# Kernel optimization log

Measured on AMD Instinct MI355X. Metric: run time of the kernel, lower is better.

## Reference

```python
import jax, jax.numpy as jnp
import numpy as np

INPUT_SIZE = 2048
HIDDEN_SIZE = 2048
BATCH = 8192


def setup_inputs() -> dict:
    key = jax.random.key(0)
    ks = jax.random.split(key, 8)
    comb = INPUT_SIZE + HIDDEN_SIZE
    s = 1.0 / np.sqrt(comb)  # torch nn.Linear default init scale
    x = jax.random.normal(ks[0], (BATCH, INPUT_SIZE), dtype=jnp.float32)
    h_prev = jax.random.normal(ks[1], (BATCH, HIDDEN_SIZE), dtype=jnp.float32)
    W_z = jax.random.uniform(ks[2], (comb, HIDDEN_SIZE), minval=-s, maxval=s, dtype=jnp.float32)
    b_z = jax.random.uniform(ks[3], (HIDDEN_SIZE,), minval=-s, maxval=s, dtype=jnp.float32)
    W_r = jax.random.uniform(ks[4], (comb, HIDDEN_SIZE), minval=-s, maxval=s, dtype=jnp.float32)
    b_r = jax.random.uniform(ks[5], (HIDDEN_SIZE,), minval=-s, maxval=s, dtype=jnp.float32)
    W_n = jax.random.uniform(ks[6], (comb, HIDDEN_SIZE), minval=-s, maxval=s, dtype=jnp.float32)
    b_n = jax.random.uniform(ks[7], (HIDDEN_SIZE,), minval=-s, maxval=s, dtype=jnp.float32)
    return {"x": x, "h_prev": h_prev, "W_z": W_z, "b_z": b_z,
            "W_r": W_r, "b_r": b_r, "W_n": W_n, "b_n": b_n}


def reference(x, h_prev, W_z, b_z, W_r, b_r, W_n, b_n):
    # combined = [x, h_prev]; avoid materializing concat by splitting the
    # weight matrices: W @ concat == x @ W_x + h @ W_h (same math).
    Wz_x, Wz_h = W_z[:INPUT_SIZE], W_z[INPUT_SIZE:]
    Wr_x, Wr_h = W_r[:INPUT_SIZE], W_r[INPUT_SIZE:]
    Wn_x, Wn_h = W_n[:INPUT_SIZE], W_n[INPUT_SIZE:]
    z = jax.nn.sigmoid(x @ Wz_x + h_prev @ Wz_h + b_z)
    r = jax.nn.sigmoid(x @ Wr_x + h_prev @ Wr_h + b_r)
    n = jnp.tanh(x @ Wn_x + (r * h_prev) @ Wn_h + b_n)
    h = (1.0 - z) * h_prev + z * n
    return h
```

## Files before the change

### kernel.cpp

```cpp
#include <hip/hip_runtime.h>
#include <hip/hip_bf16.h>
#include <stdint.h>

typedef unsigned short u16;
typedef __attribute__((ext_vector_type(8))) __bf16 bf16x8;
typedef __attribute__((ext_vector_type(4))) float f32x4;

#define BATCH 8192
#define HID   2048
#define COMB  4096
#define NT    64

__device__ __forceinline__ u16 f2bf(float f) {
  uint32_t u = __float_as_uint(f);
  u += 0x7fffu + ((u >> 16) & 1u);
  return (u16)(u >> 16);
}
__device__ __forceinline__ float bf2f(u16 b) {
  return __uint_as_float(((uint32_t)b) << 16);
}
__device__ __forceinline__ float fsigmoid(float x) { return 1.0f / (1.0f + __expf(-x)); }
__device__ __forceinline__ float ftanh(float x) { return 1.0f - 2.0f / (__expf(2.0f * x) + 1.0f); }

__device__ __forceinline__ void gload_lds16(const void* g, void* l) {
  __builtin_amdgcn_global_load_lds(
      (__attribute__((address_space(1))) void*)(uintptr_t)g,
      (__attribute__((address_space(3))) void*)(uintptr_t)l,
      16, 0, 0);
}

#define BARRIER() do { asm volatile("" ::: "memory"); __builtin_amdgcn_s_barrier(); asm volatile("" ::: "memory"); } while (0)
#define LGKM0()   asm volatile("s_waitcnt lgkmcnt(0)" ::: "memory")
#define VM6()     asm volatile("s_waitcnt vmcnt(6)" ::: "memory")
#define VM0()     asm volatile("s_waitcnt vmcnt(0)" ::: "memory")

__device__ __forceinline__ void stage_half(const u16* __restrict__ src, size_t ld,
                                           char* ldsHalf, int w, int l) {
  const int lrow = l >> 3;
  const int g    = (l & 7) ^ (lrow & 7);
#pragma unroll
  for (int i = 0; i < 2; ++i) {
    const int r0 = (w * 2 + i) * 8;
    gload_lds16(src + (size_t)(r0 + lrow) * ld + g * 8, ldsHalf + r0 * 128);
  }
}

__device__ __forceinline__ bf16x8 rd(const char* buf, int row, int kk) {
  const int byte = row * 128 + ((((kk >> 3) & 7) ^ (row & 7)) << 4);
  return *(const bf16x8*)(buf + byte);
}

#define MFMA_QUAD(MH, NH)                                                          \
  {                                                                                \
    _Pragma("unroll") for (int m_ = 0; m_ < 4; ++m_) {                             \
      _Pragma("unroll") for (int n_ = 0; n_ < 2; ++n_) {                           \
        _Pragma("unroll") for (int ks_ = 0; ks_ < 2; ++ks_) {                      \
          acc[(MH)*4 + m_][(NH)*2 + n_] = __builtin_amdgcn_mfma_f32_16x16x32_bf16( \
              af[(MH)*4 + m_][ks_], bb[(NH)*2 + n_][ks_],                          \
              acc[(MH)*4 + m_][(NH)*2 + n_], 0, 0, 0);                             \
        } } }                                                                      \
  }

__global__ void pack_A_kernel(const float* __restrict__ x, const float* __restrict__ h,
                              u16* __restrict__ A1) {
  const size_t tid = (size_t)blockIdx.x * blockDim.x + threadIdx.x;
  const int r  = (int)(tid >> 9);
  const int c8 = (int)(tid & 511);
  const float* s = (c8 < 256) ? (x + (size_t)r * 2048 + (size_t)c8 * 8)
                              : (h + (size_t)r * 2048 + (size_t)(c8 - 256) * 8);
  const float4 v0 = ((const float4*)s)[0];
  const float4 v1 = ((const float4*)s)[1];
  const uint32_t p0 = (uint32_t)f2bf(v0.x) | ((uint32_t)f2bf(v0.y) << 16);
  const uint32_t p1 = (uint32_t)f2bf(v0.z) | ((uint32_t)f2bf(v0.w) << 16);
  const uint32_t p2 = (uint32_t)f2bf(v1.x) | ((uint32_t)f2bf(v1.y) << 16);
  const uint32_t p3 = (uint32_t)f2bf(v1.z) | ((uint32_t)f2bf(v1.w) << 16);
  *(uint4*)(A1 + tid * 8) = make_uint4(p0, p1, p2, p3);
}

__global__ void transpose_w_kernel(const float* __restrict__ src, u16* __restrict__ dst) {
  __shared__ float tile[32][33];
  const int n0 = blockIdx.x * 32;
  const int k0 = blockIdx.y * 32;
  const int tx = threadIdx.x, ty = threadIdx.y;
#pragma unroll
  for (int i = 0; i < 32; i += 8)
    tile[ty + i][tx] = src[(size_t)(k0 + ty + i) * 2048 + n0 + tx];
  __syncthreads();
#pragma unroll
  for (int i = 0; i < 32; i += 8)
    dst[(size_t)(n0 + ty + i) * 4096 + k0 + tx] = f2bf(tile[tx][ty + i]);
}

template <int MODE>
__global__ __launch_bounds__(512, 2) void gemm8p_kernel(
    const u16* __restrict__ A1, const u16* __restrict__ RH,
    const u16* __restrict__ Bt, const float* __restrict__ h_prev,
    const float* __restrict__ bias0, const float* __restrict__ bias1,
    u16* __restrict__ Z, u16* __restrict__ RHout, float* __restrict__ out) {
  extern __shared__ char smem[];
  constexpr int NBN = (MODE == 0) ? 16 : 8;

  const int t = threadIdx.x;
  const int l = t & 63, w = t >> 6;
  const int wm = w >> 2, wn = w & 3;
  const int lr = l & 15, khi = l >> 4;

  const int nwg = 32 * NBN;
  int bid = blockIdx.x;
  bid = (bid & 7) * (nwg >> 3) + (bid >> 3);
  const int bm = bid / NBN, bn = bid % NBN;
  const int arow = bm * 256;
  const int brow = bn * 256;

  char* Abase = smem;
  char* Bbase = smem + 65536;

  auto stageA = [&](int T, int half) {
    const u16* src;
    size_t ld;
    if constexpr (MODE == 1) {
      if (T >= 32) { src = RH + (size_t)(arow + half * 128) * HID + (T * 64 - 2048); ld = HID; }
      else         { src = A1 + (size_t)(arow + half * 128) * COMB + T * 64;         ld = COMB; }
    } else {
      src = A1 + (size_t)(arow + half * 128) * COMB + T * 64; ld = COMB;
    }
    stage_half(src, ld, Abase + (((T & 1) * 2 + half) << 14), w, l);
  };
  auto stageB = [&](int T, int half) {
    stage_half(Bt + (size_t)(brow + half * 128) * COMB + T * 64, COMB,
               Bbase + (((T & 1) * 2 + half) << 14), w, l);
  };

  stageA(0, 0); stageA(0, 1); stageB(0, 0); stageB(0, 1);
  stageA(1, 0); stageA(1, 1); stageB(1, 0);
  VM6();
  BARRIER();

  f32x4 acc[8][4] = {};
  bf16x8 af[8][2], bb[4][2];

#pragma unroll 2
  for (int j = 0; j < NT; ++j) {
    const int p = j & 1;
    const char* Ah = Abase + (((p << 1) + wm) << 14);
    const char* Bh = Bbase + (((p << 1) + (wn >> 1)) << 14);
    const int bro = (wn & 1) * 64;

#pragma unroll
    for (int m = 0; m < 8; ++m)
#pragma unroll
      for (int ks = 0; ks < 2; ++ks)
        af[m][ks] = rd(Ah, m * 16 + lr, ks * 32 + khi * 8);
#pragma unroll
    for (int n = 0; n < 2; ++n)
#pragma unroll
      for (int ks = 0; ks < 2; ++ks)
        bb[n][ks] = rd(Bh, bro + n * 16 + lr, ks * 32 + khi * 8);
    if (j < NT - 1) stageB(j + 1, 1);
    BARRIER();
    LGKM0();
    __builtin_amdgcn_s_setprio(1);
    MFMA_QUAD(0, 0);
    __builtin_amdgcn_s_setprio(0);
    BARRIER();

    if (j < NT - 2) stageA(j + 2, 0);
    BARRIER();
    __builtin_amdgcn_s_setprio(1);
    MFMA_QUAD(1, 0);
    __builtin_amdgcn_s_setprio(0);
    BARRIER();

#pragma unroll
    for (int n = 2; n < 4; ++n)
#pragma unroll
      for (int ks = 0; ks < 2; ++ks)
        bb[n][ks] = rd(Bh, bro + n * 16 + lr, ks * 32 + khi * 8);
    if (j < NT - 2) stageA(j + 2, 1);
    BARRIER();
    LGKM0();
    __builtin_amdgcn_s_setprio(1);
    MFMA_QUAD(1, 1);
    __builtin_amdgcn_s_setprio(0);
    BARRIER();

    if (j < NT - 2) stageB(j + 2, 0);
    BARRIER();
    __builtin_amdgcn_s_setprio(1);
    MFMA_QUAD(0, 1);
    __builtin_amdgcn_s_setprio(0);
    if (j < NT - 2) { VM6(); } else { VM0(); }
    BARRIER();
  }

  const int r0g = arow + wm * 128 + khi * 4;
  const int c0g = brow + wn * 64 + lr;
  if constexpr (MODE == 0) {
    const bool isZ = (bn < 8);
    const float* bias = isZ ? bias0 : bias1;
#pragma unroll
    for (int n = 0; n < 4; ++n) {
      const int colg = c0g + n * 16;
      const int col = isZ ? colg : (colg - 2048);
      const float bv = bias[col];
#pragma unroll
      for (int m = 0; m < 8; ++m)
#pragma unroll
        for (int r = 0; r < 4; ++r) {
          const int row = r0g + m * 16 + r;
          const size_t idx = (size_t)row * HID + col;
          const float v = acc[m][n][r] + bv;
          if (isZ) {
            Z[idx] = f2bf(fsigmoid(v));
          } else {
            const float rv = fsigmoid(v);
            RHout[idx] = f2bf(rv * h_prev[idx]);
          }
        }
    }
  } else {
#pragma unroll
    for (int n = 0; n < 4; ++n) {
      const int col = c0g + n * 16;
      const float bv = bias0[col];
#pragma unroll
      for (int m = 0; m < 8; ++m)
#pragma unroll
        for (int r = 0; r < 4; ++r) {
          const int row = r0g + m * 16 + r;
          const size_t idx = (size_t)row * HID + col;
          const float nn = ftanh(acc[m][n][r] + bv);
          const float zz = bf2f(Z[idx]);
          const float hp = h_prev[idx];
          out[idx] = (1.0f - zz) * hp + zz * nn;
        }
    }
  }
}

extern "C" void kernel_launch(void* const* d_in, const int* in_sizes, int n_in,
                              void* d_out, int out_size, void* d_ws, size_t ws_size,
                              hipStream_t stream) {
  const float* x  = (const float*)d_in[0];
  const float* h  = (const float*)d_in[1];
  const float* Wz = (const float*)d_in[2];
  const float* bz = (const float*)d_in[3];
  const float* Wr = (const float*)d_in[4];
  const float* br = (const float*)d_in[5];
  const float* Wn = (const float*)d_in[6];
  const float* bn = (const float*)d_in[7];
  float* out = (float*)d_out;

  char* ws = (char*)d_ws;
  u16* A1  = (u16*)(ws);
  u16* RH  = (u16*)(ws + 67108864);
  u16* B1t = (u16*)(ws + 100663296);
  u16* B2t = (u16*)(ws + 134217728);
  u16* Z   = (u16*)(ws + 150994944);

  (void)hipFuncSetAttribute(reinterpret_cast<const void*>(&gemm8p_kernel<0>),
                            hipFuncAttributeMaxDynamicSharedMemorySize, 131072);
  (void)hipFuncSetAttribute(reinterpret_cast<const void*>(&gemm8p_kernel<1>),
                            hipFuncAttributeMaxDynamicSharedMemorySize, 131072);

  pack_A_kernel<<<16384, 256, 0, stream>>>(x, h, A1);
  dim3 tb(32, 8);
  transpose_w_kernel<<<dim3(64, 128), tb, 0, stream>>>(Wz, B1t);
  transpose_w_kernel<<<dim3(64, 128), tb, 0, stream>>>(Wr, B1t + (size_t)2048 * 4096);
  transpose_w_kernel<<<dim3(64, 128), tb, 0, stream>>>(Wn, B2t);

  gemm8p_kernel<0><<<dim3(512), 512, 131072, stream>>>(A1, nullptr, B1t, h, bz, br, Z, RH, nullptr);
  gemm8p_kernel<1><<<dim3(256), 512, 131072, stream>>>(A1, RH, B2t, h, bn, nullptr, Z, nullptr, out);
}
```

Measured before the change: 581.5 us.

## Prefetch next-tile LDS fragments during MFMA and relax waitcnts in GEMM loop

Restructures the main GEMM loop so A and B fragments for the next k-tile are read from LDS while MFMAs on the current tile run, using split lo/hi register fragments and a peeled final iteration. The loop now waits on lgkmcnt(8) rather than lgkmcnt(0), and global-to-LDS staging is reordered with finer vmcnt waits. Addressing is simplified by precomputing swizzled lane offsets. The aim is to hide LDS read latency behind matrix work, at the cost of more live registers and tighter synchronisation that could introduce races.

```diff
diff --git a/kernel.cpp b/kernel.cpp
--- a/kernel.cpp
+++ b/kernel.cpp
@@ -30,9 +30,10 @@
 }
 
 #define BARRIER() do { asm volatile("" ::: "memory"); __builtin_amdgcn_s_barrier(); asm volatile("" ::: "memory"); } while (0)
-#define LGKM0()   asm volatile("s_waitcnt lgkmcnt(0)" ::: "memory")
-#define VM6()     asm volatile("s_waitcnt vmcnt(6)" ::: "memory")
-#define VM0()     asm volatile("s_waitcnt vmcnt(0)" ::: "memory")
+#define LGKM8()   asm volatile("s_waitcnt lgkmcnt(8)" ::: "memory")
+#define VMCNT2()  asm volatile("s_waitcnt vmcnt(2)" ::: "memory")
+#define VMCNT0()  asm volatile("s_waitcnt vmcnt(0)" ::: "memory")
+#define VMCNT6()  asm volatile("s_waitcnt vmcnt(6)" ::: "memory")
 
 __device__ __forceinline__ void stage_half(const u16* __restrict__ src, size_t ld,
                                            char* ldsHalf, int w, int l) {
@@ -45,21 +46,16 @@
   }
 }
 
-__device__ __forceinline__ bf16x8 rd(const char* buf, int row, int kk) {
-  const int byte = row * 128 + ((((kk >> 3) & 7) ^ (row & 7)) << 4);
-  return *(const bf16x8*)(buf + byte);
-}
-
-#define MFMA_QUAD(MH, NH)                                                          \
-  {                                                                                \
-    _Pragma("unroll") for (int m_ = 0; m_ < 4; ++m_) {                             \
-      _Pragma("unroll") for (int n_ = 0; n_ < 2; ++n_) {                           \
-        _Pragma("unroll") for (int ks_ = 0; ks_ < 2; ++ks_) {                      \
-          acc[(MH)*4 + m_][(NH)*2 + n_] = __builtin_amdgcn_mfma_f32_16x16x32_bf16( \
-              af[(MH)*4 + m_][ks_], bb[(NH)*2 + n_][ks_],                          \
-              acc[(MH)*4 + m_][(NH)*2 + n_], 0, 0, 0);                             \
-        } } }                                                                      \
-  }
+#define RDA(base, m, ks) (*(const bf16x8*)((base) + ((ks) ? loff1 : loff0) + (m) * 2048))
+#define RDB(base, n, ks) (*(const bf16x8*)((base) + ((ks) ? loff1 : loff0) + (n) * 2048))
+
+#define MFMA_HALF(AF, BB, MH, NH)                                                     \
+  { _Pragma("unroll") for (int m_ = 0; m_ < 4; ++m_) {                                \
+      _Pragma("unroll") for (int n_ = 0; n_ < 2; ++n_) {                              \
+        _Pragma("unroll") for (int k_ = 0; k_ < 2; ++k_) {                            \
+          acc[(MH) * 4 + m_][(NH) * 2 + n_] = __builtin_amdgcn_mfma_f32_16x16x32_bf16(\
+              AF[m_][k_], BB[n_][k_], acc[(MH) * 4 + m_][(NH) * 2 + n_], 0, 0, 0);    \
+        } } } }
 
 __global__ void pack_A_kernel(const float* __restrict__ x, const float* __restrict__ h,
                               u16* __restrict__ A1) {
@@ -131,67 +127,79 @@
                Bbase + (((T & 1) * 2 + half) << 14), w, l);
   };
 
+  const int loff0 = lr * 128 + (((khi)     ^ (lr & 7)) << 4);
+  const int loff1 = lr * 128 + (((4 + khi) ^ (lr & 7)) << 4);
+  const char* A0p = Abase + ((0 * 2 + wm) << 14);
+  const char* A1p = Abase + ((1 * 2 + wm) << 14);
+  const char* B0p = Bbase + ((0 * 2 + (wn >> 1)) << 14) + (wn & 1) * 64 * 128;
+  const char* B1p = Bbase + ((1 * 2 + (wn >> 1)) << 14) + (wn & 1) * 64 * 128;
+
   stageA(0, 0); stageA(0, 1); stageB(0, 0); stageB(0, 1);
-  stageA(1, 0); stageA(1, 1); stageB(1, 0);
-  VM6();
+  stageB(1, 0); stageB(1, 1); stageA(1, 0);
+  VMCNT6();
   BARRIER();
 
   f32x4 acc[8][4] = {};
-  bf16x8 af[8][2], bb[4][2];
+  bf16x8 af_lo[4][2], af_hi[4][2], bb_lo[2][2], bb_hi[2][2];
+
+#pragma unroll
+  for (int m = 0; m < 4; ++m) { af_lo[m][0] = RDA(A0p, m, 0); af_lo[m][1] = RDA(A0p, m, 1); }
+#pragma unroll
+  for (int n = 0; n < 2; ++n) { bb_hi[n][0] = RDB(B0p, n + 2, 0); bb_hi[n][1] = RDB(B0p, n + 2, 1); }
+#pragma unroll
+  for (int n = 0; n < 2; ++n) { bb_lo[n][0] = RDB(B0p, n, 0); bb_lo[n][1] = RDB(B0p, n, 1); }
 
 #pragma unroll 2
-  for (int j = 0; j < NT; ++j) {
-    const int p = j & 1;
-    const char* Ah = Abase + (((p << 1) + wm) << 14);
-    const char* Bh = Bbase + (((p << 1) + (wn >> 1)) << 14);
-    const int bro = (wn & 1) * 64;
-
-#pragma unroll
-    for (int m = 0; m < 8; ++m)
-#pragma unroll
-      for (int ks = 0; ks < 2; ++ks)
-        af[m][ks] = rd(Ah, m * 16 + lr, ks * 32 + khi * 8);
-#pragma unroll
-    for (int n = 0; n < 2; ++n)
-#pragma unroll
-      for (int ks = 0; ks < 2; ++ks)
-        bb[n][ks] = rd(Bh, bro + n * 16 + lr, ks * 32 + khi * 8);
-    if (j < NT - 1) stageB(j + 1, 1);
-    BARRIER();
-    LGKM0();
-    __builtin_amdgcn_s_setprio(1);
-    MFMA_QUAD(0, 0);
+  for (int j = 0; j < NT - 1; ++j) {
+    const bool odd = j & 1;
+    const char* Acur = odd ? A1p : A0p;
+    const char* Anxt = odd ? A0p : A1p;
+    const char* Bnxt = odd ? B0p : B1p;
+
+    stageA(j + 1, 1);
+    BARRIER();
+#pragma unroll
+    for (int m = 0; m < 4; ++m) { af_hi[m][0] = RDA(Acur, m + 4, 0); af_hi[m][1] = RDA(Acur, m + 4, 1); }
+    __builtin_amdgcn_s_setprio(1);
+    MFMA_HALF(af_lo, bb_lo, 0, 0);
+    __builtin_amdgcn_s_setprio(0);
+    LGKM8();
+    BARRIER();
+
+    if (j < NT - 2) stageB(j + 2, 0);
+    BARRIER();
+    __builtin_amdgcn_s_setprio(1);
+    MFMA_HALF(af_lo, bb_hi, 0, 1);
+    __builtin_amdgcn_s_setprio(0);
+    BARRIER();
+
+    if (j < NT - 2) { VMCNT2(); stageB(j + 2, 1); } else { VMCNT0(); }
+    BARRIER();
+#pragma unroll
+    for (int m = 0; m < 4; ++m) { af_lo[m][0] = RDA(Anxt, m, 0); af_lo[m][1] = RDA(Anxt, m, 1); }
+    __builtin_amdgcn_s_setprio(1);
+    MFMA_HALF(af_hi, bb_hi, 1, 1);
     __builtin_amdgcn_s_setprio(0);
     BARRIER();
 
     if (j < NT - 2) stageA(j + 2, 0);
     BARRIER();
-    __builtin_amdgcn_s_setprio(1);
-    MFMA_QUAD(1, 0);
-    __builtin_amdgcn_s_setprio(0);
-    BARRIER();
-
-#pragma unroll
-    for (int n = 2; n < 4; ++n)
-#pragma unroll
-      for (int ks = 0; ks < 2; ++ks)
-        bb[n][ks] = rd(Bh, bro + n * 16 + lr, ks * 32 + khi * 8);
-    if (j < NT - 2) stageA(j + 2, 1);
-    BARRIER();
-    LGKM0();
-    __builtin_amdgcn_s_setprio(1);
-    MFMA_QUAD(1, 1);
-    __builtin_amdgcn_s_setprio(0);
-    BARRIER();
-
-    if (j < NT - 2) stageB(j + 2, 0);
-    BARRIER();
-    __builtin_amdgcn_s_setprio(1);
-    MFMA_QUAD(0, 1);
-    __builtin_amdgcn_s_setprio(0);
-    if (j < NT - 2) { VM6(); } else { VM0(); }
+#pragma unroll
+    for (int n = 0; n < 2; ++n) { bb_hi[n][0] = RDB(Bnxt, n + 2, 0); bb_hi[n][1] = RDB(Bnxt, n + 2, 1); }
+    __builtin_amdgcn_s_setprio(1);
+    MFMA_HALF(af_hi, bb_lo, 1, 0);
+    __builtin_amdgcn_s_setprio(0);
+#pragma unroll
+    for (int n = 0; n < 2; ++n) { bb_lo[n][0] = RDB(Bnxt, n, 0); bb_lo[n][1] = RDB(Bnxt, n, 1); }
     BARRIER();
   }
+
+#pragma unroll
+  for (int m = 0; m < 4; ++m) { af_hi[m][0] = RDA(A1p, m + 4, 0); af_hi[m][1] = RDA(A1p, m + 4, 1); }
+  MFMA_HALF(af_lo, bb_lo, 0, 0);
+  MFMA_HALF(af_lo, bb_hi, 0, 1);
+  MFMA_HALF(af_hi, bb_hi, 1, 1);
+  MFMA_HALF(af_hi, bb_lo, 1, 0);
 
   const int r0g = arow + wm * 128 + khi * 4;
   const int c0g = brow + wn * 64 + lr;
```

After: 679.0 us. 1.17x slower.

## Split A-fragment LDS reads and A staging across MFMA phases with precomputed offsets

Applied to the files above, without the earlier changes.

The LDS reads of the A fragments are split so half are loaded before the first MFMA quad and half before the second, rather than all up front. The A global-to-LDS staging is reissued as quarter-tile loads, spread over two phases and covering both halves, instead of whole halves in separate phases. Swizzled LDS offsets are precomputed once per thread, and a partial lgkmcnt wait is added before the first barrier. The aim is to spread LDS and VMEM traffic more evenly across the MFMA phases and cut address arithmetic, at the cost of reordering which buffer regions are written when, which could risk hazards or extra stalls.

```diff
diff --git a/kernel.cpp b/kernel.cpp
--- a/kernel.cpp
+++ b/kernel.cpp
@@ -31,6 +31,7 @@
 
 #define BARRIER() do { asm volatile("" ::: "memory"); __builtin_amdgcn_s_barrier(); asm volatile("" ::: "memory"); } while (0)
 #define LGKM0()   asm volatile("s_waitcnt lgkmcnt(0)" ::: "memory")
+#define LGKM8()   asm volatile("s_waitcnt lgkmcnt(8)" ::: "memory")
 #define VM6()     asm volatile("s_waitcnt vmcnt(6)" ::: "memory")
 #define VM0()     asm volatile("s_waitcnt vmcnt(0)" ::: "memory")
 
@@ -45,9 +46,12 @@
   }
 }
 
-__device__ __forceinline__ bf16x8 rd(const char* buf, int row, int kk) {
-  const int byte = row * 128 + ((((kk >> 3) & 7) ^ (row & 7)) << 4);
-  return *(const bf16x8*)(buf + byte);
+__device__ __forceinline__ void stage_q(const u16* __restrict__ src, size_t ld,
+                                        char* ldsHalf, int q, int w, int l) {
+  const int lrow = l >> 3;
+  const int g    = (l & 7) ^ (lrow & 7);
+  const int r0   = q * 64 + w * 8;
+  gload_lds16(src + (size_t)(r0 + lrow) * ld + g * 8, ldsHalf + r0 * 128);
 }
 
 #define MFMA_QUAD(MH, NH)                                                          \
@@ -115,24 +119,31 @@
   char* Abase = smem;
   char* Bbase = smem + 65536;
 
-  auto stageA = [&](int T, int half) {
-    const u16* src;
-    size_t ld;
+  auto asrc = [&](int T, int half) -> const u16* {
     if constexpr (MODE == 1) {
-      if (T >= 32) { src = RH + (size_t)(arow + half * 128) * HID + (T * 64 - 2048); ld = HID; }
-      else         { src = A1 + (size_t)(arow + half * 128) * COMB + T * 64;         ld = COMB; }
-    } else {
-      src = A1 + (size_t)(arow + half * 128) * COMB + T * 64; ld = COMB;
-    }
-    stage_half(src, ld, Abase + (((T & 1) * 2 + half) << 14), w, l);
+      if (T >= 32) return RH + (size_t)(arow + half * 128) * HID + (T * 64 - 2048);
+    }
+    return A1 + (size_t)(arow + half * 128) * COMB + T * 64;
+  };
+  auto ald = [&](int T) -> size_t {
+    if constexpr (MODE == 1) { if (T >= 32) return HID; }
+    return COMB;
+  };
+  auto stageAq = [&](int T, int half, int q) {
+    stage_q(asrc(T, half), ald(T), Abase + (((T & 1) * 2 + half) << 14), q, w, l);
   };
   auto stageB = [&](int T, int half) {
     stage_half(Bt + (size_t)(brow + half * 128) * COMB + T * 64, COMB,
                Bbase + (((T & 1) * 2 + half) << 14), w, l);
   };
 
-  stageA(0, 0); stageA(0, 1); stageB(0, 0); stageB(0, 1);
-  stageA(1, 0); stageA(1, 1); stageB(1, 0);
+  const int loff0 = lr * 128 + ((khi       ^ (lr & 7)) << 4);
+  const int loff1 = lr * 128 + (((4 + khi) ^ (lr & 7)) << 4);
+
+  stageAq(0, 0, 0); stageAq(0, 1, 0); stageAq(0, 0, 1); stageAq(0, 1, 1);
+  stageB(0, 0); stageB(0, 1);
+  stageAq(1, 0, 0); stageAq(1, 1, 0); stageAq(1, 0, 1); stageAq(1, 1, 1);
+  stageB(1, 0);
   VM6();
   BARRIER();
 
@@ -143,20 +154,20 @@
   for (int j = 0; j < NT; ++j) {
     const int p = j & 1;
     const char* Ah = Abase + (((p << 1) + wm) << 14);
-    const char* Bh = Bbase + (((p << 1) + (wn >> 1)) << 14);
-    const int bro = (wn & 1) * 64;
-
-#pragma unroll
-    for (int m = 0; m < 8; ++m)
-#pragma unroll
-      for (int ks = 0; ks < 2; ++ks)
-        af[m][ks] = rd(Ah, m * 16 + lr, ks * 32 + khi * 8);
-#pragma unroll
-    for (int n = 0; n < 2; ++n)
-#pragma unroll
-      for (int ks = 0; ks < 2; ++ks)
-        bb[n][ks] = rd(Bh, bro + n * 16 + lr, ks * 32 + khi * 8);
+    const char* Bh = Bbase + (((p << 1) + (wn >> 1)) << 14) + (wn & 1) * 64 * 128;
+
+#pragma unroll
+    for (int m = 0; m < 4; ++m) {
+      af[m][0] = *(const bf16x8*)(Ah + m * 2048 + loff0);
+      af[m][1] = *(const bf16x8*)(Ah + m * 2048 + loff1);
+    }
+#pragma unroll
+    for (int n = 0; n < 2; ++n) {
+      bb[n][0] = *(const bf16x8*)(Bh + n * 2048 + loff0);
+      bb[n][1] = *(const bf16x8*)(Bh + n * 2048 + loff1);
+    }
     if (j < NT - 1) stageB(j + 1, 1);
+    LGKM8();
     BARRIER();
     LGKM0();
     __builtin_amdgcn_s_setprio(1);
@@ -164,19 +175,25 @@
     __builtin_amdgcn_s_setprio(0);
     BARRIER();
 
-    if (j < NT - 2) stageA(j + 2, 0);
-    BARRIER();
+#pragma unroll
+    for (int m = 4; m < 8; ++m) {
+      af[m][0] = *(const bf16x8*)(Ah + m * 2048 + loff0);
+      af[m][1] = *(const bf16x8*)(Ah + m * 2048 + loff1);
+    }
+    if (j < NT - 2) { stageAq(j + 2, 0, 0); stageAq(j + 2, 1, 0); }
+    BARRIER();
+    LGKM0();
     __builtin_amdgcn_s_setprio(1);
     MFMA_QUAD(1, 0);
     __builtin_amdgcn_s_setprio(0);
     BARRIER();
 
 #pragma unroll
-    for (int n = 2; n < 4; ++n)
-#pragma unroll
-      for (int ks = 0; ks < 2; ++ks)
-        bb[n][ks] = rd(Bh, bro + n * 16 + lr, ks * 32 + khi * 8);
-    if (j < NT - 2) stageA(j + 2, 1);
+    for (int n = 2; n < 4; ++n) {
+      bb[n][0] = *(const bf16x8*)(Bh + n * 2048 + loff0);
+      bb[n][1] = *(const bf16x8*)(Bh + n * 2048 + loff1);
+    }
+    if (j < NT - 2) { stageAq(j + 2, 0, 1); stageAq(j + 2, 1, 1); }
     BARRIER();
     LGKM0();
     __builtin_amdgcn_s_setprio(1);
```

New measurement: 579.4 us. About the same (-0.3%).

## Replace 256x256 ping-pong GEMM with 256x128 triple-buffered K=32 pipeline

Applied to the files above, without the earlier changes.

Rewrites the main bf16 GEMM kernel to use 256x128 output tiles, a K step of 32 and three rotating LDS buffers, with one barrier per iteration instead of several interleaved sub-phases. Per-wave accumulators drop from 8x4 to 4x4 MFMA tiles, LDS use falls to 72 KB and launch bounds rise to allow more resident blocks. This aims at higher occupancy and simpler synchronisation, at the cost of lower arithmetic intensity per tile and more global traffic for the shared B and A operands.

```diff
diff --git a/kernel.cpp b/kernel.cpp
--- a/kernel.cpp
+++ b/kernel.cpp
@@ -9,7 +9,7 @@
 #define BATCH 8192
 #define HID   2048
 #define COMB  4096
-#define NT    64
+#define NTT   128
 
 __device__ __forceinline__ u16 f2bf(float f) {
   uint32_t u = __float_as_uint(f);
@@ -30,36 +30,8 @@
 }
 
 #define BARRIER() do { asm volatile("" ::: "memory"); __builtin_amdgcn_s_barrier(); asm volatile("" ::: "memory"); } while (0)
-#define LGKM0()   asm volatile("s_waitcnt lgkmcnt(0)" ::: "memory")
-#define VM6()     asm volatile("s_waitcnt vmcnt(6)" ::: "memory")
+#define VM3()     asm volatile("s_waitcnt vmcnt(3)" ::: "memory")
 #define VM0()     asm volatile("s_waitcnt vmcnt(0)" ::: "memory")
-
-__device__ __forceinline__ void stage_half(const u16* __restrict__ src, size_t ld,
-                                           char* ldsHalf, int w, int l) {
-  const int lrow = l >> 3;
-  const int g    = (l & 7) ^ (lrow & 7);
-#pragma unroll
-  for (int i = 0; i < 2; ++i) {
-    const int r0 = (w * 2 + i) * 8;
-    gload_lds16(src + (size_t)(r0 + lrow) * ld + g * 8, ldsHalf + r0 * 128);
-  }
-}
-
-__device__ __forceinline__ bf16x8 rd(const char* buf, int row, int kk) {
-  const int byte = row * 128 + ((((kk >> 3) & 7) ^ (row & 7)) << 4);
-  return *(const bf16x8*)(buf + byte);
-}
-
-#define MFMA_QUAD(MH, NH)                                                          \
-  {                                                                                \
-    _Pragma("unroll") for (int m_ = 0; m_ < 4; ++m_) {                             \
-      _Pragma("unroll") for (int n_ = 0; n_ < 2; ++n_) {                           \
-        _Pragma("unroll") for (int ks_ = 0; ks_ < 2; ++ks_) {                      \
-          acc[(MH)*4 + m_][(NH)*2 + n_] = __builtin_amdgcn_mfma_f32_16x16x32_bf16( \
-              af[(MH)*4 + m_][ks_], bb[(NH)*2 + n_][ks_],                          \
-              acc[(MH)*4 + m_][(NH)*2 + n_], 0, 0, 0);                             \
-        } } }                                                                      \
-  }
 
 __global__ void pack_A_kernel(const float* __restrict__ x, const float* __restrict__ h,
                               u16* __restrict__ A1) {
@@ -92,17 +64,17 @@
 }
 
 template <int MODE>
-__global__ __launch_bounds__(512, 2) void gemm8p_kernel(
+__global__ __launch_bounds__(512, 4) void gemm3b_kernel(
     const u16* __restrict__ A1, const u16* __restrict__ RH,
     const u16* __restrict__ Bt, const float* __restrict__ h_prev,
     const float* __restrict__ bias0, const float* __restrict__ bias1,
     u16* __restrict__ Z, u16* __restrict__ RHout, float* __restrict__ out) {
   extern __shared__ char smem[];
-  constexpr int NBN = (MODE == 0) ? 16 : 8;
+  constexpr int NBN = (MODE == 0) ? 32 : 16;
 
   const int t = threadIdx.x;
   const int l = t & 63, w = t >> 6;
-  const int wm = w >> 2, wn = w & 3;
+  const int wm = w >> 1, wn = w & 1;
   const int lr = l & 15, khi = l >> 4;
 
   const int nwg = 32 * NBN;
@@ -110,93 +82,73 @@
   bid = (bid & 7) * (nwg >> 3) + (bid >> 3);
   const int bm = bid / NBN, bn = bid % NBN;
   const int arow = bm * 256;
-  const int brow = bn * 256;
-
-  char* Abase = smem;
-  char* Bbase = smem + 65536;
-
-  auto stageA = [&](int T, int half) {
+  const int brow = bn * 128;
+
+  const int sr   = l >> 2;
+  const int gsrc = (l & 3) ^ ((sr >> 1) & 3);
+
+  auto stageA = [&](int T, char* slot) {
     const u16* src;
     size_t ld;
+    int koff;
     if constexpr (MODE == 1) {
-      if (T >= 32) { src = RH + (size_t)(arow + half * 128) * HID + (T * 64 - 2048); ld = HID; }
-      else         { src = A1 + (size_t)(arow + half * 128) * COMB + T * 64;         ld = COMB; }
+      if (T >= 64) { src = RH; ld = HID;  koff = T * 32 - 2048; }
+      else         { src = A1; ld = COMB; koff = T * 32; }
     } else {
-      src = A1 + (size_t)(arow + half * 128) * COMB + T * 64; ld = COMB;
+      src = A1; ld = COMB; koff = T * 32;
     }
-    stage_half(src, ld, Abase + (((T & 1) * 2 + half) << 14), w, l);
+#pragma unroll
+    for (int i = 0; i < 2; ++i)
+      gload_lds16(src + (size_t)(arow + i * 128 + w * 16 + sr) * ld + koff + gsrc * 8,
+                  slot + i * 8192 + w * 1024);
   };
-  auto stageB = [&](int T, int half) {
-    stage_half(Bt + (size_t)(brow + half * 128) * COMB + T * 64, COMB,
-               Bbase + (((T & 1) * 2 + half) << 14), w, l);
+  auto stageB = [&](int T, char* slot) {
+    gload_lds16(Bt + (size_t)(brow + w * 16 + sr) * COMB + T * 32 + gsrc * 8,
+                slot + w * 1024);
   };
 
-  stageA(0, 0); stageA(0, 1); stageB(0, 0); stageB(0, 1);
-  stageA(1, 0); stageA(1, 1); stageB(1, 0);
-  VM6();
+  const int loff = lr * 64 + ((khi ^ ((lr >> 1) & 3)) << 4);
+
+  char* As0 = smem;          char* As1 = smem + 16384;  char* As2 = smem + 32768;
+  char* Bs0 = smem + 49152;  char* Bs1 = smem + 57344;  char* Bs2 = smem + 65536;
+
+  stageA(0, As0); stageB(0, Bs0);
+  stageA(1, As1); stageB(1, Bs1);
+  VM3();
   BARRIER();
 
-  f32x4 acc[8][4] = {};
-  bf16x8 af[8][2], bb[4][2];
-
-#pragma unroll 2
-  for (int j = 0; j < NT; ++j) {
-    const int p = j & 1;
-    const char* Ah = Abase + (((p << 1) + wm) << 14);
-    const char* Bh = Bbase + (((p << 1) + (wn >> 1)) << 14);
-    const int bro = (wn & 1) * 64;
-
-#pragma unroll
-    for (int m = 0; m < 8; ++m)
-#pragma unroll
-      for (int ks = 0; ks < 2; ++ks)
-        af[m][ks] = rd(Ah, m * 16 + lr, ks * 32 + khi * 8);
-#pragma unroll
-    for (int n = 0; n < 2; ++n)
-#pragma unroll
-      for (int ks = 0; ks < 2; ++ks)
-        bb[n][ks] = rd(Bh, bro + n * 16 + lr, ks * 32 + khi * 8);
-    if (j < NT - 1) stageB(j + 1, 1);
-    BARRIER();
-    LGKM0();
+  f32x4 acc[4][4] = {};
+
+  for (int j = 0; j < NTT; ++j) {
+    if (j < NTT - 2) { stageA(j + 2, As2); stageB(j + 2, Bs2); }
+
+    bf16x8 af[4], bb[4];
+#pragma unroll
+    for (int m = 0; m < 4; ++m)
+      af[m] = *(const bf16x8*)(As0 + wm * 4096 + m * 1024 + loff);
+#pragma unroll
+    for (int n = 0; n < 4; ++n)
+      bb[n] = *(const bf16x8*)(Bs0 + wn * 4096 + n * 1024 + loff);
+
     __builtin_amdgcn_s_setprio(1);
-    MFMA_QUAD(0, 0);
+#pragma unroll
+    for (int m = 0; m < 4; ++m)
+#pragma unroll
+      for (int n = 0; n < 4; ++n)
+        acc[m][n] = __builtin_amdgcn_mfma_f32_16x16x32_bf16(af[m], bb[n], acc[m][n], 0, 0, 0);
     __builtin_amdgcn_s_setprio(0);
-    BARRIER();
-
-    if (j < NT - 2) stageA(j + 2, 0);
-    BARRIER();
-    __builtin_amdgcn_s_setprio(1);
-    MFMA_QUAD(1, 0);
-    __builtin_amdgcn_s_setprio(0);
-    BARRIER();
-
-#pragma unroll
-    for (int n = 2; n < 4; ++n)
-#pragma unroll
-      for (int ks = 0; ks < 2; ++ks)
-        bb[n][ks] = rd(Bh, bro + n * 16 + lr, ks * 32 + khi * 8);
-    if (j < NT - 2) stageA(j + 2, 1);
-    BARRIER();
-    LGKM0();
-    __builtin_amdgcn_s_setprio(1);
-    MFMA_QUAD(1, 1);
-    __builtin_amdgcn_s_setprio(0);
-    BARRIER();
-
-    if (j < NT - 2) stageB(j + 2, 0);
-    BARRIER();
-    __builtin_amdgcn_s_setprio(1);
-    MFMA_QUAD(0, 1);
-    __builtin_amdgcn_s_setprio(0);
-    if (j < NT - 2) { VM6(); } else { VM0(); }
-    BARRIER();
+
+    if (j < NTT - 2) { VM3(); } else if (j == NTT - 2) { VM0(); }
+    if (j < NTT - 1) BARRIER();
+
+    char* ta = As0; As0 = As1; As1 = As2; As2 = ta;
+    char* tb = Bs0; Bs0 = Bs1; Bs1 = Bs2; Bs2 = tb;
   }
 
-  const int r0g = arow + wm * 128 + khi * 4;
-  const int c0g = brow + wn * 64 + lr;
+  const int r0g = arow + wm * 64 + khi * 4;
   if constexpr (MODE == 0) {
-    const bool isZ = (bn < 8);
+    const bool isZ = (bn < 16);
+    const int c0g = bn * 128 + wn * 64 + lr;
     const float* bias = isZ ? bias0 : bias1;
 #pragma unroll
     for (int n = 0; n < 4; ++n) {
@@ -204,7 +156,7 @@
       const int col = isZ ? colg : (colg - 2048);
       const float bv = bias[col];
 #pragma unroll
-      for (int m = 0; m < 8; ++m)
+      for (int m = 0; m < 4; ++m)
 #pragma unroll
         for (int r = 0; r < 4; ++r) {
           const int row = r0g + m * 16 + r;
@@ -219,12 +171,13 @@
         }
     }
   } else {
+    const int c0g = bn * 128 + wn * 64 + lr;
 #pragma unroll
     for (int n = 0; n < 4; ++n) {
       const int col = c0g + n * 16;
       const float bv = bias0[col];
 #pragma unroll
-      for (int m = 0; m < 8; ++m)
+      for (int m = 0; m < 4; ++m)
 #pragma unroll
         for (int r = 0; r < 4; ++r) {
           const int row = r0g + m * 16 + r;
@@ -258,10 +211,10 @@
   u16* B2t = (u16*)(ws + 134217728);
   u16* Z   = (u16*)(ws + 150994944);
 
-  (void)hipFuncSetAttribute(reinterpret_cast<const void*>(&gemm8p_kernel<0>),
-                            hipFuncAttributeMaxDynamicSharedMemorySize, 131072);
-  (void)hipFuncSetAttribute(reinterpret_cast<const void*>(&gemm8p_kernel<1>),
-                            hipFuncAttributeMaxDynamicSharedMemorySize, 131072);
+  (void)hipFuncSetAttribute(reinterpret_cast<const void*>(&gemm3b_kernel<0>),
+                            hipFuncAttributeMaxDynamicSharedMemorySize, 73728);
+  (void)hipFuncSetAttribute(reinterpret_cast<const void*>(&gemm3b_kernel<1>),
+                            hipFuncAttributeMaxDynamicSharedMemorySize, 73728);
 
   pack_A_kernel<<<16384, 256, 0, stream>>>(x, h, A1);
   dim3 tb(32, 8);
@@ -269,6 +222,6 @@
   transpose_w_kernel<<<dim3(64, 128), tb, 0, stream>>>(Wr, B1t + (size_t)2048 * 4096);
   transpose_w_kernel<<<dim3(64, 128), tb, 0, stream>>>(Wn, B2t);
 
-  gemm8p_kernel<0><<<dim3(512), 512, 131072, stream>>>(A1, nullptr, B1t, h, bz, br, Z, RH, nullptr);
-  gemm8p_kernel<1><<<dim3(256), 512, 131072, stream>>>(A1, RH, B2t, h, bn, nullptr, Z, nullptr, out);
-}
+  gemm3b_kernel<0><<<dim3(1024), 512, 73728, stream>>>(A1, nullptr, B1t, h, bz, br, Z, RH, nullptr);
+  gemm3b_kernel<1><<<dim3(512), 512, 73728, stream>>>(A1, RH, B2t, h, bn, nullptr, Z, nullptr, out);
+}
```

Result: slower. 597.6 us (+2.8%).
